# Kernel tuning notes

Measured on AMD Instinct MI355X. Metric: run time of the kernel, lower is better.

Reference implementation:

```python
import jax, jax.numpy as jnp
import numpy as np

EPSILON = 0.1      # privacy parameter
GUMBEL_EPS = 1e-10 # uniform clamp used by sample_gumbel
NORM_EPS = 1e-12   # F.normalize denominator clamp

V, D = 50257, 768
B, T = 2, 1024


def _l2_normalize(x):
    # matches torch F.normalize(p=2, dim=-1): x / max(||x||, 1e-12)
    n = jnp.linalg.norm(x, axis=-1, keepdims=True)
    return x / jnp.maximum(n, NORM_EPS)


def setup_inputs() -> dict:
    key = jax.random.key(0)
    k1, k2, k3 = jax.random.split(key, 3)
    weight = jax.random.normal(k1, (V, D), dtype=jnp.float32)
    input_ids = jax.random.randint(k2, (B, T), 0, V, dtype=jnp.int64)
    gumbel_u = jax.random.uniform(
        k3, (B * T, V), dtype=jnp.float32,
        minval=GUMBEL_EPS, maxval=1.0 - GUMBEL_EPS)
    return {"input_ids": input_ids, "weight": weight, "gumbel_u": gumbel_u}


def reference(input_ids, weight, gumbel_u):
    Bi, Ti = input_ids.shape
    Dw = weight.shape[1]
    vectors = weight[input_ids]                      # (B, T, D) embedding lookup
    vecs_n = _l2_normalize(vectors.reshape(Bi * Ti, Dw))  # (BT, D)
    embed_n = _l2_normalize(weight)                  # (V, D)
    similarity = vecs_n @ embed_n.T                  # (BT, V) cosine sims
    gumbel = -jnp.log(-jnp.log(gumbel_u))            # Gumbel(0,1) noise
    noisy_scores = similarity + (2.0 / EPSILON) * gumbel
    selected = jnp.argmax(noisy_scores, axis=1)      # (BT,)
    return weight[selected].reshape(Bi, Ti, Dw)      # gather original embeddings
```

## Files before the change

### kernel.cpp

```cpp
#include <hip/hip_runtime.h>
#include <math.h>


constexpr int V  = 50257;
constexpr int D  = 768;
constexpr int BT = 2048;
constexpr long TOTAL = (long)BT * V;
constexpr int ITOTAL = (int)TOTAL;
constexpr int NF4    = ITOTAL >> 2;
constexpr int LOG2C  = 12;
constexpr int WCHUNK = 1 << LOG2C;
constexpr int NWC    = (ITOTAL + WCHUNK - 1) / WCHUNK;
constexpr int CCAP   = 16;
constexpr float KPOW = 1.1052847f;
constexpr float TWO_OVER_EPS = 20.0f;

typedef float f32x4 __attribute__((ext_vector_type(4)));

__global__ __launch_bounds__(256) void k_scan(const float* __restrict__ gum,
                                              int* __restrict__ ccnt,
                                              int* __restrict__ cflat,
                                              float* __restrict__ cuv) {
  int tid  = threadIdx.x;
  int lane = tid & 63;
  int wc   = blockIdx.x * 4 + (tid >> 6);
  if (wc >= NWC) return;

  int start  = wc * WCHUNK;
  int row0   = start / V;
  int bnd    = (row0 + 1) * V;
  int f4base = start >> 2;

  const f32x4* g4 = reinterpret_cast<const f32x4*>(gum);
  f32x4 v[16];
#pragma unroll
  for (int k = 0; k < 16; ++k) {
    int fi = f4base + k * 64 + lane;
    if (fi < NF4) v[k] = __builtin_nontemporal_load(&g4[fi]);
    else          v[k] = (f32x4){-1.f, -1.f, -1.f, -1.f};
  }

  float mlo = -1.f, mhi = -1.f;
#pragma unroll
  for (int k = 0; k < 16; ++k) {
    int e0 = (f4base + k * 64 + lane) << 2;
#pragma unroll
    for (int j = 0; j < 4; ++j) {
      if (e0 + j < bnd) mlo = fmaxf(mlo, v[k][j]);
      else              mhi = fmaxf(mhi, v[k][j]);
    }
  }
#pragma unroll
  for (int off = 1; off < 64; off <<= 1) {
    mlo = fmaxf(mlo, __shfl_xor(mlo, off, 64));
    mhi = fmaxf(mhi, __shfl_xor(mhi, off, 64));
  }
  float tlo = expf(KPOW * logf(mlo));
  float thi = expf(KPOW * logf(mhi));

  int base = 0;
#pragma unroll
  for (int k = 0; k < 16; ++k) {
    int e0 = (f4base + k * 64 + lane) << 2;
#pragma unroll
    for (int j = 0; j < 4; ++j) {
      int idx = e0 + j;
      float uu = v[k][j];
      bool pred = uu >= ((idx < bnd) ? tlo : thi);
      unsigned long long mask = __ballot(pred);
      if (pred) {
        int p = base + __popcll(mask & ((1ull << lane) - 1ull));
        if (p < CCAP) {
          cflat[wc * CCAP + p] = idx;
          cuv[wc * CCAP + p]   = uu;
        }
      }
      base += __popcll(mask);
    }
  }
  if (lane == 0) ccnt[wc] = (base < CCAP) ? base : CCAP;
}

__global__ __launch_bounds__(256) void k_score(const float* __restrict__ w,
                                               const int* __restrict__ ids,
                                               const int* __restrict__ ccnt,
                                               const int* __restrict__ cflat,
                                               const float* __restrict__ cuv,
                                               float* __restrict__ out) {
  __shared__ __align__(16) float q[D];
  __shared__ float lu[256], lsc[256];
  __shared__ int   li[256];
  __shared__ float s_red[4];
  __shared__ float s_invq;
  __shared__ int   s_n, s_sel;
  int row = blockIdx.x;
  int tid = threadIdx.x;
  int lane = tid & 63, wid = tid >> 6;

  if (tid == 0) s_n = 0;
  __syncthreads();

  int c0 = (row * V) >> LOG2C;
  int c1 = (((row + 1) * V) - 1) >> LOG2C;
  int nch = c1 - c0 + 1;
  if (tid < nch) {
    int c = c0 + tid;
    int m = ccnt[c]; if (m > CCAP) m = CCAP;
    int lo = row * V, hi = lo + V;
    for (int k = 0; k < m; ++k) {
      int fx = cflat[c * CCAP + k];
      if (fx >= lo && fx < hi) {
        int p = atomicAdd(&s_n, 1);
        if (p < 256) { li[p] = fx - lo; lu[p] = cuv[c * CCAP + k]; }
      }
    }
  }
  int qid = ids[row];
  float qs = 0.f;
#pragma unroll
  for (int k = 0; k < 3; ++k) {
    float x = w[(size_t)qid * D + k * 256 + tid];
    q[k * 256 + tid] = x;
    qs += x * x;
  }
#pragma unroll
  for (int off = 32; off > 0; off >>= 1) qs += __shfl_down(qs, off, 64);
  if (lane == 0) s_red[wid] = qs;
  __syncthreads();
  if (tid == 0)
    s_invq = 1.0f / fmaxf(sqrtf(s_red[0] + s_red[1] + s_red[2] + s_red[3]), 1e-12f);
  __syncthreads();
  float invq = s_invq;
  int n = s_n; if (n > 256) n = 256;

  for (int cI = wid; cI < n; cI += 4) {
    int j = li[cI];
    const float4* p  = reinterpret_cast<const float4*>(w + (size_t)j * D);
    const float4* qp = reinterpret_cast<const float4*>(q);
    float dot = 0.f, n2 = 0.f;
#pragma unroll
    for (int k = 0; k < 3; ++k) {
      float4 a = p[k * 64 + lane];
      float4 b = qp[k * 64 + lane];
      dot += a.x * b.x + a.y * b.y + a.z * b.z + a.w * b.w;
      n2  += a.x * a.x + a.y * a.y + a.z * a.z + a.w * a.w;
    }
#pragma unroll
    for (int off = 32; off > 0; off >>= 1) {
      dot += __shfl_down(dot, off, 64);
      n2  += __shfl_down(n2,  off, 64);
    }
    if (lane == 0) {
      float invj = 1.0f / fmaxf(sqrtf(n2), 1e-12f);
      float uu = lu[cI];
      lsc[cI] = invq * invj * dot + TWO_OVER_EPS * (-logf(-logf(uu)));
    }
  }
  __syncthreads();

  if (wid == 0) {
    float bs = -INFINITY;
    int bj = 0x7fffffff;
    for (int cI = lane; cI < n; cI += 64) {
      float s = lsc[cI];
      int j = li[cI];
      if (s > bs || (s == bs && j < bj)) { bs = s; bj = j; }
    }
#pragma unroll
    for (int off = 32; off > 0; off >>= 1) {
      float os = __shfl_down(bs, off, 64);
      int   oj = __shfl_down(bj, off, 64);
      if (os > bs || (os == bs && oj < bj)) { bs = os; bj = oj; }
    }
    if (lane == 0) s_sel = bj;
  }
  __syncthreads();

  int sel = s_sel;
#pragma unroll
  for (int k = 0; k < 3; ++k)
    out[(size_t)row * D + k * 256 + tid] = w[(size_t)sel * D + k * 256 + tid];
}

extern "C" void kernel_launch(void* const* d_in, const int* in_sizes, int n_in,
                              void* d_out, int out_size, void* d_ws, size_t ws_size,
                              hipStream_t stream) {
  const int*   ids = (const int*)d_in[0];
  const float* w   = (const float*)d_in[1];
  const float* gum = (const float*)d_in[2];
  float* out = (float*)d_out;

  char* ws = (char*)d_ws;
  int*   ccnt  = (int*)ws;
  int*   cflat = (int*)(ws + NWC * 4);
  float* cuv   = (float*)(ws + NWC * 4 + NWC * CCAP * 4);

  k_scan<<<(NWC + 3) / 4, 256, 0, stream>>>(gum, ccnt, cflat, cuv);
  k_score<<<BT, 256, 0, stream>>>(w, ids, ccnt, cflat, cuv, out);
}
```

Measured before the change: 94.73 us.

## Scan gumbel in block-wide chunks and add per-row threshold candidate filtering

The scan kernel now handles one 8192-element chunk per 256-thread block instead of one 4096-element chunk per wave. It reduces the chunk maximum across the block, stores per-chunk low and high maxima, and gathers candidates with an LDS atomic counter instead of wave ballots. The score kernel combines these chunk maxima into an exact per-row maximum and keeps only candidates that pass a tighter row-level threshold, so fewer weight rows are dot-producted. The trade-off is an extra block sync in the scan and a 16-entry cap per larger chunk, which could drop valid candidates if many pass the coarser chunk threshold.

```diff
diff --git a/kernel.cpp b/kernel.cpp
--- a/kernel.cpp
+++ b/kernel.cpp
@@ -8,11 +8,13 @@
 constexpr long TOTAL = (long)BT * V;
 constexpr int ITOTAL = (int)TOTAL;
 constexpr int NF4    = ITOTAL >> 2;
-constexpr int LOG2C  = 12;
-constexpr int WCHUNK = 1 << LOG2C;
-constexpr int NWC    = (ITOTAL + WCHUNK - 1) / WCHUNK;
+constexpr int LOG2C  = 13;
+constexpr int CHUNK  = 1 << LOG2C;
+constexpr int NBLK   = (ITOTAL + CHUNK - 1) / CHUNK;
 constexpr int CCAP   = 16;
-constexpr float KPOW = 1.1052847f;
+constexpr int RCAP   = 64;
+constexpr float KPOW_SCAN = 1.1107096f;
+constexpr float KPOW_ROW  = 1.1274969f;
 constexpr float TWO_OVER_EPS = 20.0f;
 
 typedef float f32x4 __attribute__((ext_vector_type(4)));
@@ -20,65 +22,84 @@
 __global__ __launch_bounds__(256) void k_scan(const float* __restrict__ gum,
                                               int* __restrict__ ccnt,
                                               int* __restrict__ cflat,
-                                              float* __restrict__ cuv) {
-  int tid  = threadIdx.x;
-  int lane = tid & 63;
-  int wc   = blockIdx.x * 4 + (tid >> 6);
-  if (wc >= NWC) return;
-
-  int start  = wc * WCHUNK;
-  int row0   = start / V;
-  int bnd    = (row0 + 1) * V;
+                                              float* __restrict__ cuv,
+                                              float* __restrict__ cmaxlo,
+                                              float* __restrict__ cmaxhi) {
+  __shared__ float slo[4], shi[4];
+  __shared__ float s_tlo, s_thi;
+  __shared__ int s_cnt;
+  int tid = threadIdx.x, b = blockIdx.x;
+  int lane = tid & 63, wid = tid >> 6;
+  int start = b * CHUNK;
+  int end = start + CHUNK; if (end > ITOTAL) end = ITOTAL;
+  int row0 = start / V;
+  int bnd  = (row0 + 1) * V;
+  bool hasHi = end > bnd;
+
+  if (tid == 0) s_cnt = 0;
+
+  const f32x4* g4 = reinterpret_cast<const f32x4*>(gum);
   int f4base = start >> 2;
-
-  const f32x4* g4 = reinterpret_cast<const f32x4*>(gum);
-  f32x4 v[16];
-#pragma unroll
-  for (int k = 0; k < 16; ++k) {
-    int fi = f4base + k * 64 + lane;
+  f32x4 v[8];
+#pragma unroll
+  for (int k = 0; k < 8; ++k) {
+    int fi = f4base + k * 256 + tid;
     if (fi < NF4) v[k] = __builtin_nontemporal_load(&g4[fi]);
     else          v[k] = (f32x4){-1.f, -1.f, -1.f, -1.f};
   }
 
   float mlo = -1.f, mhi = -1.f;
-#pragma unroll
-  for (int k = 0; k < 16; ++k) {
-    int e0 = (f4base + k * 64 + lane) << 2;
-#pragma unroll
-    for (int j = 0; j < 4; ++j) {
-      if (e0 + j < bnd) mlo = fmaxf(mlo, v[k][j]);
-      else              mhi = fmaxf(mhi, v[k][j]);
-    }
+  if (hasHi) {
+#pragma unroll
+    for (int k = 0; k < 8; ++k) {
+      int e0 = (f4base + k * 256 + tid) << 2;
+#pragma unroll
+      for (int j = 0; j < 4; ++j) {
+        if (e0 + j < bnd) mlo = fmaxf(mlo, v[k][j]);
+        else              mhi = fmaxf(mhi, v[k][j]);
+      }
+    }
+  } else {
+#pragma unroll
+    for (int k = 0; k < 8; ++k)
+#pragma unroll
+      for (int j = 0; j < 4; ++j) mlo = fmaxf(mlo, v[k][j]);
   }
 #pragma unroll
   for (int off = 1; off < 64; off <<= 1) {
     mlo = fmaxf(mlo, __shfl_xor(mlo, off, 64));
     mhi = fmaxf(mhi, __shfl_xor(mhi, off, 64));
   }
-  float tlo = expf(KPOW * logf(mlo));
-  float thi = expf(KPOW * logf(mhi));
-
-  int base = 0;
-#pragma unroll
-  for (int k = 0; k < 16; ++k) {
-    int e0 = (f4base + k * 64 + lane) << 2;
+  if (lane == 0) { slo[wid] = mlo; shi[wid] = mhi; }
+  __syncthreads();
+  if (tid == 0) {
+    float a = fmaxf(fmaxf(slo[0], slo[1]), fmaxf(slo[2], slo[3]));
+    float c = fmaxf(fmaxf(shi[0], shi[1]), fmaxf(shi[2], shi[3]));
+    cmaxlo[b] = a;
+    cmaxhi[b] = c;
+    s_tlo = expf(KPOW_SCAN * logf(a));
+    s_thi = expf(KPOW_SCAN * logf(c));
+  }
+  __syncthreads();
+  float tlo = s_tlo, thi = s_thi;
+#pragma unroll
+  for (int k = 0; k < 8; ++k) {
+    int e0 = (f4base + k * 256 + tid) << 2;
 #pragma unroll
     for (int j = 0; j < 4; ++j) {
       int idx = e0 + j;
       float uu = v[k][j];
-      bool pred = uu >= ((idx < bnd) ? tlo : thi);
-      unsigned long long mask = __ballot(pred);
-      if (pred) {
-        int p = base + __popcll(mask & ((1ull << lane) - 1ull));
+      if (uu >= ((idx < bnd) ? tlo : thi)) {
+        int p = atomicAdd(&s_cnt, 1);
         if (p < CCAP) {
-          cflat[wc * CCAP + p] = idx;
-          cuv[wc * CCAP + p]   = uu;
+          cflat[b * CCAP + p] = idx;
+          cuv[b * CCAP + p]   = uu;
         }
       }
-      base += __popcll(mask);
-    }
-  }
-  if (lane == 0) ccnt[wc] = (base < CCAP) ? base : CCAP;
+    }
+  }
+  __syncthreads();
+  if (tid == 0) ccnt[b] = (s_cnt < CCAP) ? s_cnt : CCAP;
 }
 
 __global__ __launch_bounds__(256) void k_score(const float* __restrict__ w,
@@ -86,52 +107,64 @@
                                                const int* __restrict__ ccnt,
                                                const int* __restrict__ cflat,
                                                const float* __restrict__ cuv,
+                                               const float* __restrict__ cmaxlo,
+                                               const float* __restrict__ cmaxhi,
                                                float* __restrict__ out) {
   __shared__ __align__(16) float q[D];
-  __shared__ float lu[256], lsc[256];
-  __shared__ int   li[256];
-  __shared__ float s_red[4];
-  __shared__ float s_invq;
+  __shared__ float lu[RCAP], lsc[RCAP];
+  __shared__ int   li[RCAP];
+  __shared__ float s_rm[8], s_red[4];
+  __shared__ float s_ut, s_invq;
   __shared__ int   s_n, s_sel;
   int row = blockIdx.x;
   int tid = threadIdx.x;
   int lane = tid & 63, wid = tid >> 6;
 
-  if (tid == 0) s_n = 0;
-  __syncthreads();
-
   int c0 = (row * V) >> LOG2C;
   int c1 = (((row + 1) * V) - 1) >> LOG2C;
   int nch = c1 - c0 + 1;
+  if (tid == 0) s_n = 0;
+  if (tid < nch) {
+    int c = c0 + tid;
+    int row0c = (c * CHUNK) / V;
+    s_rm[tid] = (row0c == row) ? cmaxlo[c] : cmaxhi[c];
+  }
+  int qid = ids[row];
+  float qs = 0.f;
+#pragma unroll
+  for (int k = 0; k < 3; ++k) {
+    float x = w[(size_t)qid * D + k * 256 + tid];
+    q[k * 256 + tid] = x;
+    qs += x * x;
+  }
+#pragma unroll
+  for (int off = 32; off > 0; off >>= 1) qs += __shfl_down(qs, off, 64);
+  if (lane == 0) s_red[wid] = qs;
+  __syncthreads();
+  if (tid == 0) {
+    float rm = -1.f;
+    for (int k = 0; k < nch; ++k) rm = fmaxf(rm, s_rm[k]);
+    s_ut = expf(KPOW_ROW * logf(rm));
+    s_invq = 1.0f / fmaxf(sqrtf(s_red[0] + s_red[1] + s_red[2] + s_red[3]), 1e-12f);
+  }
+  __syncthreads();
+  float ut = s_ut, invq = s_invq;
+
   if (tid < nch) {
     int c = c0 + tid;
     int m = ccnt[c]; if (m > CCAP) m = CCAP;
     int lo = row * V, hi = lo + V;
     for (int k = 0; k < m; ++k) {
       int fx = cflat[c * CCAP + k];
-      if (fx >= lo && fx < hi) {
+      float uu = cuv[c * CCAP + k];
+      if (fx >= lo && fx < hi && uu >= ut) {
         int p = atomicAdd(&s_n, 1);
-        if (p < 256) { li[p] = fx - lo; lu[p] = cuv[c * CCAP + k]; }
+        if (p < RCAP) { li[p] = fx - lo; lu[p] = uu; }
       }
     }
   }
-  int qid = ids[row];
-  float qs = 0.f;
-#pragma unroll
-  for (int k = 0; k < 3; ++k) {
-    float x = w[(size_t)qid * D + k * 256 + tid];
-    q[k * 256 + tid] = x;
-    qs += x * x;
-  }
-#pragma unroll
-  for (int off = 32; off > 0; off >>= 1) qs += __shfl_down(qs, off, 64);
-  if (lane == 0) s_red[wid] = qs;
-  __syncthreads();
-  if (tid == 0)
-    s_invq = 1.0f / fmaxf(sqrtf(s_red[0] + s_red[1] + s_red[2] + s_red[3]), 1e-12f);
-  __syncthreads();
-  float invq = s_invq;
-  int n = s_n; if (n > 256) n = 256;
+  __syncthreads();
+  int n = s_n; if (n > RCAP) n = RCAP;
 
   for (int cI = wid; cI < n; cI += 4) {
     int j = li[cI];
@@ -152,8 +185,7 @@
     }
     if (lane == 0) {
       float invj = 1.0f / fmaxf(sqrtf(n2), 1e-12f);
-      float uu = lu[cI];
-      lsc[cI] = invq * invj * dot + TWO_OVER_EPS * (-logf(-logf(uu)));
+      lsc[cI] = invq * invj * dot + TWO_OVER_EPS * (-logf(-logf(lu[cI])));
     }
   }
   __syncthreads();
@@ -190,11 +222,18 @@
   const float* gum = (const float*)d_in[2];
   float* out = (float*)d_out;
 
+  constexpr size_t O_CCNT = 0;
+  constexpr size_t O_MLO  = O_CCNT + (size_t)NBLK * 4;
+  constexpr size_t O_MHI  = O_MLO  + (size_t)NBLK * 4;
+  constexpr size_t O_CFL  = O_MHI  + (size_t)NBLK * 4;
+  constexpr size_t O_CUV  = O_CFL  + (size_t)NBLK * CCAP * 4;
   char* ws = (char*)d_ws;
-  int*   ccnt  = (int*)ws;
-  int*   cflat = (int*)(ws + NWC * 4);
-  float* cuv   = (float*)(ws + NWC * 4 + NWC * CCAP * 4);
-
-  k_scan<<<(NWC + 3) / 4, 256, 0, stream>>>(gum, ccnt, cflat, cuv);
-  k_score<<<BT, 256, 0, stream>>>(w, ids, ccnt, cflat, cuv, out);
+  int*   ccnt   = (int*)(ws + O_CCNT);
+  float* cmaxlo = (float*)(ws + O_MLO);
+  float* cmaxhi = (float*)(ws + O_MHI);
+  int*   cflat  = (int*)(ws + O_CFL);
+  float* cuv    = (float*)(ws + O_CUV);
+
+  k_scan<<<NBLK, 256, 0, stream>>>(gum, ccnt, cflat, cuv, cmaxlo, cmaxhi);
+  k_score<<<BT, 256, 0, stream>>>(w, ids, ccnt, cflat, cuv, cmaxlo, cmaxhi, out);
 }
```

New measurement: 78.70 us. -16.9%, faster.
